# Kernel optimization log

Measured on AMD Instinct MI355X. Metric: run time of the kernel, lower is better.

The kernel has to match this reference:

```python
import jax, jax.numpy as jnp
import numpy as np
from jax import lax

B, HCH, NCODES, H, W = 16, 32, 256, 256, 256

def conv2d(x, w, b, pad):
    y = lax.conv_general_dilated(x, w, (1, 1), [(pad, pad), (pad, pad)],
                                 dimension_numbers=('NCHW', 'OIHW', 'NCHW'))
    return y + b[None, :, None, None]

def vq(z, codebook):
    # z: (B,C,H,W); codebook: (K,C)
    zf = jnp.transpose(z, (0, 2, 3, 1)).reshape(-1, z.shape[1])  # (BHW,C)
    dists = (zf ** 2).sum(1, keepdims=True) + (codebook ** 2).sum(1) - 2.0 * zf @ codebook.T
    idx = jnp.argmin(dists, axis=1)
    zq = codebook[idx].reshape(z.shape[0], z.shape[2], z.shape[3], z.shape[1])
    zq = jnp.transpose(zq, (0, 3, 1, 2))
    # straight-through estimator
    return z + lax.stop_gradient(zq - z)

def setup_inputs() -> dict:
    key = jax.random.key(0)
    ks = jax.random.split(key, 12)
    s = lambda k, shp, scale=0.1: (jax.random.normal(k, shp, jnp.float32) * scale)
    return {
        'x': jax.random.normal(ks[0], (B, 1, H, W), jnp.float32),
        'stem_w': s(ks[1], (HCH, 1, 3, 3)),
        'stem_b': s(ks[2], (HCH,)),
        'up1_w': s(ks[3], (HCH, HCH, 3, 3)),
        'up1_b': s(ks[4], (HCH,)),
        'up2_w': s(ks[5], (HCH, HCH, 1, 1)),
        'up2_b': s(ks[6], (HCH,)),
        'tau_w': s(ks[7], (HCH, HCH, 1, 1)),
        'tau_b': s(ks[8], (HCH,)),
        'codebook': jax.random.uniform(ks[9], (NCODES, HCH), jnp.float32,
                                       -1.0 / NCODES, 1.0 / NCODES),
        'dec_w': s(ks[10], (1, HCH, 1, 1)),
        'dec_b': s(ks[11], (1,)),
        'n_steps': 5,
    }

def reference(x, stem_w, stem_b, up1_w, up1_b, up2_w, up2_b, tau_w, tau_b,
              codebook, dec_w, dec_b, n_steps):
    state = jax.nn.relu(conv2d(x, stem_w, stem_b, 1))
    for t in range(n_steps):
        delta = conv2d(jax.nn.relu(conv2d(state, up1_w, up1_b, 1)), up2_w, up2_b, 0)
        beta = jax.nn.sigmoid(conv2d(state, tau_w, tau_b, 0))
        state = beta * state + (1.0 - beta) * delta
        state = vq(state, codebook)  # vq_every = 1
    return jax.nn.sigmoid(conv2d(state, dec_w, dec_b, 0))
```

## Files before the change

### kernel.cpp

```cpp
#include <hip/hip_runtime.h>
#include <hip/hip_bf16.h>

#define BATCH 16
#define HH 256
#define WW 256
#define NPIX (BATCH*HH*WW)
#define NSTEPS 5
#define CBS 40
#define HS  258
#define HIMG (HS*HS)

#define W1P 0
#define W2P 9216
#define WTP 10240
#define IDP 11264
#define CBP 12288
#define FRAGS_TOT 20480

using u16 = unsigned short;
using u32 = unsigned int;
using u8  = unsigned char;

typedef __attribute__((ext_vector_type(8))) short bf8_t;
typedef __attribute__((ext_vector_type(4))) float f4_t;

#define MFMA16 __builtin_amdgcn_mfma_f32_16x16x32_bf16

#define DPPMIN(v, CTRL) do { \
    u32 _o = (u32)__builtin_amdgcn_update_dpp((int)(v), (int)(v), (CTRL), 0xF, 0xF, false); \
    (v) = _o < (v) ? _o : (v); } while (0)

#define LDS_ORDER() asm volatile("" ::: "memory")

__device__ __forceinline__ float bf2f(u32 u) {
    union { u32 i; float f; } v; v.i = u << 16; return v.f;
}
__device__ __forceinline__ u16 f2bf(float f) {
    union { float f; u32 i; } v; v.f = f;
    u32 x = v.i;
    x += 0x7fffu + ((x >> 16) & 1u);
    return (u16)(x >> 16);
}
__device__ __forceinline__ u32 pack2bf(float a, float b) {
    __hip_bfloat162 h2 = __float22bfloat162_rn(float2{a, b});
    union { __hip_bfloat162 h; u32 u; } v; v.h = h2; return v.u;
}
__device__ __forceinline__ float ldin(const void* p, int i, int f32) {
    return f32 ? ((const float*)p)[i] : bf2f(((const u16*)p)[i]);
}
__device__ __forceinline__ u16 ldbf(const void* p, int i, int f32) {
    return f32 ? f2bf(((const float*)p)[i]) : ((const u16*)p)[i];
}
__device__ __forceinline__ int sniff_f32(const void* xraw) {
    const u32* xw = (const u32*)xraw;
    int cnt = 0;
    for (int j = 0; j < 64; j++) {
        u32 w = xw[j];
        float flo = bf2f(w & 0xffffu);
        float a = fabsf(flo);
        if (flo == 0.0f || (a >= 6e-8f && a <= 64.0f)) cnt++;
    }
    return (cnt < 32) ? 1 : 0;
}
__device__ __forceinline__ int chperm(int kp) { return (kp >> 1) | ((kp & 1) << 4); }

__global__ void prep_kernel(const void* x,
    const void* stem_w, const void* stem_b, const void* up1_w, const void* up1_b,
    const void* up2_w, const void* up2_b, const void* tau_w, const void* tau_b,
    const void* cb, const void* dec_w, const void* dec_b,
    u16* frags, u16* cb_bf, u16* idxh_a, u16* idxh_b,
    float* cn2, float* cadj, float* decdot, float* wf0,
    float* up1_bf, float* up2_bf, float* tau_bf, float* stem_bf, int* flag)
{
    int f32 = sniff_f32(x);
    int i = blockIdx.x * 256 + threadIdx.x;
    if (i == 0) *flag = f32;
    if (i < 9216) {
        int slot = i >> 9, rem = i & 511, lane = rem >> 3, j = rem & 7;
        int tap = slot >> 1, nt = slot & 1;
        int co = nt*16 + (lane & 15), ci = chperm((lane >> 4)*8 + j);
        frags[W1P + i] = ldbf(up1_w, (co*32+ci)*9 + tap, f32);
        return;
    }
    i -= 9216;
    if (i < 1024) {
        int nt = i >> 9, rem = i & 511, lane = rem >> 3, j = rem & 7;
        int co = nt*16 + (lane & 15), k = chperm((lane >> 4)*8 + j);
        frags[W2P + i] = f2bf(-0.25f * ldin(up2_w, co*32 + k, f32));
        return;
    }
    i -= 1024;
    if (i < 1024) {
        int nt = i >> 9, rem = i & 511, lane = rem >> 3, j = rem & 7;
        int co = nt*16 + (lane & 15), k = chperm((lane >> 4)*8 + j);
        frags[WTP + i] = ldbf(tau_w, co*32 + k, f32);
        return;
    }
    i -= 1024;
    if (i < 1024) {
        int s = i >> 9, rem = i & 511, lane = rem >> 3, j = rem & 7;
        int colq = lane & 15, quad = lane >> 4;
        int ch = chperm(quad*8 + j);
        frags[IDP + i] = (ch == (colq + s*16)) ? (u16)0xBE80 : (u16)0;
        return;
    }
    i -= 1024;
    if (i < 8192) {
        int nt = i >> 9, rem = i & 511, lane = rem >> 3, j = rem & 7;
        int code = nt*16 + (lane & 15), c = chperm((lane >> 4)*8 + j);
        frags[CBP + i] = ldbf(cb, code*32 + c, f32);
        return;
    }
    i -= 8192;
    if (i < 257*CBS) {
        int row = i / CBS, p = i - row*CBS;
        cb_bf[i] = (p < 32 && row < 256) ? ldbf(cb, row*32 + chperm(p), f32) : (u16)0;
        return;
    }
    i -= 257*CBS;
    if (i < 16448) {
        int bb = i / 1028, r = i - bb*1028;
        int row, colh;
        if (r < 258)      { row = 0;            colh = r; }
        else if (r < 516) { row = 257;          colh = r - 258; }
        else if (r < 774) { row = r - 516 + 1;  colh = 0; }
        else              { row = r - 774 + 1;  colh = 257; }
        int a = bb*HIMG + row*HS + colh;
        idxh_a[a] = 256; idxh_b[a] = 256;
        return;
    }
    i -= 16448;
    if (i < 256) {
        float s = 0.f;
        for (int c = 0; c < 32; c++) { float v = ldin(cb, i*32+c, f32); s += v*v; }
        cn2[i] = 0.5f * s;
        return;
    }
    i -= 256;
    if (i < 256) {
        float s = 0.f;
        for (int c = 0; c < 32; c++) { float v = ldin(cb, i*32+c, f32); s += v*v; }
        cadj[i] = 0.25f * (0.5f * s) + 0.5f;
        return;
    }
    i -= 256;
    if (i < 256) {
        float s = ldin(dec_b, 0, f32);
        for (int c = 0; c < 32; c++) s += ldin(dec_w, c, f32) * ldin(cb, i*32+c, f32);
        decdot[i] = s;
        return;
    }
    i -= 256;
    if (i < 288) {
        int tap = i >> 5, co = i & 31;
        wf0[i] = ldin(stem_w, co*9 + tap, f32);
        return;
    }
    i -= 288;
    if (i < 32) { up1_bf[i]  = ldin(up1_b, i, f32); return; }
    i -= 32;
    if (i < 32) { up2_bf[i]  = -0.25f * ldin(up2_b, i, f32); return; }
    i -= 32;
    if (i < 32) { tau_bf[i]  = ldin(tau_b, i, f32); return; }
    i -= 32;
    if (i < 32) { stem_bf[i] = ldin(stem_b, i, f32); return; }
}

__global__ __launch_bounds__(256) void step0_kernel(
    const void* __restrict__ xraw, const int* __restrict__ flagp,
    u16* __restrict__ idx_out,
    const u16* __restrict__ fragsg, const float* __restrict__ cn2,
    const float* __restrict__ up1_b, const float* __restrict__ up2_b,
    const float* __restrict__ tau_b, const float* __restrict__ wf0,
    const float* __restrict__ stem_bf)
{
    __shared__ __align__(16) u16 smem[23680];
    u16* w1f   = smem;
    u16* w2f   = smem + 9216;
    u16* wtf   = smem + 10240;
    u16* tileq = smem + 11264;
    u16* hzb   = smem + 21632;
    float* xs  = (float*)hzb;

    const u16* __restrict__ cbg = fragsg + CBP;

    int tid = threadIdx.x;
    int lane = tid & 63, wave = tid >> 6;
    int col = lane & 15, quad = lane >> 4;
    int b = blockIdx.z, x0 = blockIdx.x * 16, y0 = blockIdx.y * 16;

    bf8_t id0 = *(const bf8_t*)&fragsg[IDP + (0*64+lane)*8];
    bf8_t id1 = *(const bf8_t*)&fragsg[IDP + (1*64+lane)*8];

    {
        const uint4* s4 = (const uint4*)(fragsg + W1P);
        uint4* d4 = (uint4*)smem;
        for (int i = tid; i < 1408; i += 256) d4[i] = s4[i];
    }

    {
        int f32 = *flagp;
        for (int pp = tid; pp < 400; pp += 256) {
            int r = pp / 20, c = pp - r*20;
            int gy = y0 - 2 + r, gx = x0 - 2 + c;
            float v = 0.f;
            if ((unsigned)gy < 256u && (unsigned)gx < 256u)
                v = ldin(xraw, (b << 16) | (gy << 8) | gx, f32);
            xs[pp] = v;
        }
        __syncthreads();
        for (int pp = tid; pp < 324; pp += 256) {
            int r = pp / 18, c = pp - r*18;
            int gy = y0 - 1 + r, gx = x0 - 1 + c;
            uint4 qv[4] = {{0,0,0,0},{0,0,0,0},{0,0,0,0},{0,0,0,0}};
            if ((unsigned)gy < 256u && (unsigned)gx < 256u) {
                float acc[32];
#pragma unroll
                for (int co = 0; co < 32; co++) acc[co] = stem_bf[co];
#pragma unroll
                for (int tap = 0; tap < 9; tap++) {
                    float v = xs[(r + tap/3)*20 + (c + tap%3)];
                    const float* w = &wf0[tap*32];
#pragma unroll
                    for (int co = 0; co < 32; co++) acc[co] = fmaf(v, w[co], acc[co]);
                }
                u32* ow = (u32*)qv;
#pragma unroll
                for (int m = 0; m < 16; m++)
                    ow[m] = pack2bf(fmaxf(acc[m], 0.f), fmaxf(acc[m+16], 0.f));
            }
#pragma unroll
            for (int q = 0; q < 4; q++)
                *(uint4*)&tileq[(q*324 + pp)*8] = qv[q];
        }
    }
    __syncthreads();

    float cn2adj[16];
#pragma unroll
    for (int nt = 0; nt < 16; nt++) cn2adj[nt] = 0.25f*cn2[nt*16+col] + 0.5f;
    float bu1C0 = up1_b[col], bu1C1 = up1_b[col+16];
    float bu2_0 = up2_b[col], bu2_1 = up2_b[col+16];
    float bt0 = tau_b[col],   bt1 = tau_b[col+16];
    u16* hzw = &hzb[wave*512];
    u32* hz32 = (u32*)hzw;
    int wy = wave * 4;
    f4_t kz = {0.f,0.f,0.f,0.f};

    bf8_t rows[4][3];
#pragma unroll
    for (int i = 0; i < 4; i++)
#pragma unroll
        for (int dx = 0; dx < 3; dx++)
            rows[i][dx] = *(const bf8_t*)&tileq[(quad*324 + (wy+i)*18 + col+dx)*8];

#pragma unroll
    for (int rrp = 0; rrp < 2; rrp++) {
        if (rrp) {
#pragma unroll
            for (int dx = 0; dx < 3; dx++) {
                rows[0][dx] = rows[2][dx];
                rows[1][dx] = rows[3][dx];
                rows[2][dx] = *(const bf8_t*)&tileq[(quad*324 + (wy+4)*18 + col+dx)*8];
                rows[3][dx] = *(const bf8_t*)&tileq[(quad*324 + (wy+5)*18 + col+dx)*8];
            }
        }
        f4_t aA0 = kz, aA1 = kz, aB0 = kz, aB1 = kz;
#pragma unroll
        for (int t = 0; t < 9; t++) {
            int dy = t/3, dx = t - dy*3;
            bf8_t wA = *(const bf8_t*)&w1f[((t*2+0)*64 + lane)*8];
            bf8_t wB = *(const bf8_t*)&w1f[((t*2+1)*64 + lane)*8];
            aA0 = MFMA16(rows[dy  ][dx], wA, aA0, 0, 0, 0);
            aA1 = MFMA16(rows[dy  ][dx], wB, aA1, 0, 0, 0);
            aB0 = MFMA16(rows[dy+1][dx], wA, aB0, 0, 0, 0);
            aB1 = MFMA16(rows[dy+1][dx], wB, aB1, 0, 0, 0);
        }
#pragma unroll
        for (int r = 0; r < 4; r++) {
            int px = quad*4 + r;
            hz32[px*16 + col] = pack2bf(fmaxf(aA0[r] + bu1C0, 0.f),
                                        fmaxf(aA1[r] + bu1C1, 0.f));
        }
        LDS_ORDER();
        bf8_t hA0 = *(const bf8_t*)&hzw[col*32 + quad*8];
        LDS_ORDER();
#pragma unroll
        for (int r = 0; r < 4; r++) {
            int px = quad*4 + r;
            hz32[px*16 + col] = pack2bf(fmaxf(aB0[r] + bu1C0, 0.f),
                                        fmaxf(aB1[r] + bu1C1, 0.f));
        }
        LDS_ORDER();
        bf8_t hA1 = *(const bf8_t*)&hzw[col*32 + quad*8];
        LDS_ORDER();

        bf8_t w20 = *(const bf8_t*)&w2f[(0*64+lane)*8];
        bf8_t w21 = *(const bf8_t*)&w2f[(1*64+lane)*8];
        bf8_t wt0 = *(const bf8_t*)&wtf[(0*64+lane)*8];
        bf8_t wt1 = *(const bf8_t*)&wtf[(1*64+lane)*8];
        bf8_t sA0 = rows[1][1], sA1 = rows[2][1];
        f4_t d00 = MFMA16(hA0, w20, kz, 0, 0, 0);
        f4_t d01 = MFMA16(hA0, w21, kz, 0, 0, 0);
        f4_t d10 = MFMA16(hA1, w20, kz, 0, 0, 0);
        f4_t d11 = MFMA16(hA1, w21, kz, 0, 0, 0);
        f4_t t00 = MFMA16(sA0, wt0, kz, 0, 0, 0);
        f4_t t01 = MFMA16(sA0, wt1, kz, 0, 0, 0);
        f4_t t10 = MFMA16(sA1, wt0, kz, 0, 0, 0);
        f4_t t11 = MFMA16(sA1, wt1, kz, 0, 0, 0);
        f4_t S0l = MFMA16(sA0, id0, kz, 0, 0, 0);
        f4_t S0h = MFMA16(sA0, id1, kz, 0, 0, 0);
        f4_t S1l = MFMA16(sA1, id0, kz, 0, 0, 0);
        f4_t S1h = MFMA16(sA1, id1, kz, 0, 0, 0);

#pragma unroll
        for (int r = 0; r < 4; r++) {
            int px = quad*4 + r;
            float dl0 = d00[r] + bu2_0, tv0 = t00[r] + bt0;
            float be0 = 1.0f / (1.0f + __expf(-tv0));
            float dl1 = d01[r] + bu2_1, tv1 = t01[r] + bt1;
            float be1 = 1.0f / (1.0f + __expf(-tv1));
            hz32[px*16 + col] = pack2bf(dl0 + be0*(S0l[r] - dl0),
                                        dl1 + be1*(S0h[r] - dl1));
        }
        LDS_ORDER();
        bf8_t zA0 = *(const bf8_t*)&hzw[col*32 + quad*8];
        LDS_ORDER();
#pragma unroll
        for (int r = 0; r < 4; r++) {
            int px = quad*4 + r;
            float dl0 = d10[r] + bu2_0, tv0 = t10[r] + bt0;
            float be0 = 1.0f / (1.0f + __expf(-tv0));
            float dl1 = d11[r] + bu2_1, tv1 = t11[r] + bt1;
            float be1 = 1.0f / (1.0f + __expf(-tv1));
            hz32[px*16 + col] = pack2bf(dl0 + be0*(S1l[r] - dl0),
                                        dl1 + be1*(S1h[r] - dl1));
        }
        LDS_ORDER();
        bf8_t zA1 = *(const bf8_t*)&hzw[col*32 + quad*8];
        LDS_ORDER();

        u32 b0[4], b1[4];
#pragma unroll
        for (int r = 0; r < 4; r++) { b0[r] = 0xFFFFFFFFu; b1[r] = 0xFFFFFFFFu; }
#pragma unroll 4
        for (int nt = 0; nt < 16; nt++) {
            bf8_t cf = *(const bf8_t*)&cbg[(nt*64 + lane)*8];
            f4_t ci = {cn2adj[nt], cn2adj[nt], cn2adj[nt], cn2adj[nt]};
            f4_t s0 = MFMA16(zA0, cf, ci, 0, 0, 0);
            f4_t s1 = MFMA16(zA1, cf, ci, 0, 0, 0);
            u32 code = (u32)(nt*16) | (u32)col;
#pragma unroll
            for (int r = 0; r < 4; r++) {
                u32 k0 = (__builtin_bit_cast(u32, s0[r]) & 0xFFFFFF00u) | code;
                u32 k1 = (__builtin_bit_cast(u32, s1[r]) & 0xFFFFFF00u) | code;
                b0[r] = k0 < b0[r] ? k0 : b0[r];
                b1[r] = k1 < b1[r] ? k1 : b1[r];
            }
        }
#pragma unroll
        for (int r = 0; r < 4; r++) {
            DPPMIN(b0[r], 0x121); DPPMIN(b0[r], 0x122);
            DPPMIN(b0[r], 0x124); DPPMIN(b0[r], 0x128);
            DPPMIN(b1[r], 0x121); DPPMIN(b1[r], 0x122);
            DPPMIN(b1[r], 0x124); DPPMIN(b1[r], 0x128);
        }
        int yr = y0 + wy + rrp*2;
        if (col < 4) {
            int xc = x0 + quad*4 + col + 1;
            idx_out[b*HIMG + (yr+1)*HS + xc] = (u16)(b0[col] & 255u);
            idx_out[b*HIMG + (yr+2)*HS + xc] = (u16)(b1[col] & 255u);
        }
    }
}

__global__ __launch_bounds__(256) void step1_kernel(
    const u16* __restrict__ idx_in, u16* __restrict__ idx_out,
    const u16* __restrict__ fragsg, const u16* __restrict__ cbr_g,
    const float* __restrict__ cadj_g,
    const float* __restrict__ up1_b, const float* __restrict__ up2_b,
    const float* __restrict__ tau_b)
{
    __shared__ __align__(16) u16 smem[24104];
    u16* w1f = smem;
    u16* w2f = smem + 9216;
    u16* wtf = smem + 10240;
    u16* cbr = smem + 11264;
    float* cadjf = (float*)(smem + 21544);
    u16* hzb = smem + 22056;

    int tid = threadIdx.x;
    int lane = tid & 63, wave = tid >> 6;
    int col = lane & 15, quad = lane >> 4;
    int b = blockIdx.z, x0 = blockIdx.x * 16, y0 = blockIdx.y * 32;
    int wy = wave * 4;

    bf8_t id0 = *(const bf8_t*)&fragsg[IDP + (0*64+lane)*8];
    bf8_t id1 = *(const bf8_t*)&fragsg[IDP + (1*64+lane)*8];

    {
        const uint4* s4 = (const uint4*)(fragsg + W1P);
        uint4* d4 = (uint4*)smem;
        for (int i = tid; i < 1408; i += 256) d4[i] = s4[i];
        const uint4* c4 = (const uint4*)cbr_g;
        uint4* e4 = (uint4*)cbr;
        for (int i = tid; i < 1285; i += 256) e4[i] = c4[i];
        const uint4* a4 = (const uint4*)cadj_g;
        uint4* f4p = (uint4*)cadjf;
        if (tid < 64) f4p[tid] = a4[tid];
    }
    __syncthreads();

    float bu1C0 = up1_b[col], bu1C1 = up1_b[col+16];
    float bu2_0 = up2_b[col], bu2_1 = up2_b[col+16];
    float bt0 = tau_b[col],   bt1 = tau_b[col+16];
    u16* hzw = &hzb[wave*512];
    u32* hz32 = (u32*)hzw;
    f4_t kz = {0.f,0.f,0.f,0.f};

    for (int th = 0; th < 2; th++) {
        int yb = y0 + th*16;

        u32 kp[6];
#pragma unroll
        for (int tr = 0; tr < 6; tr++) {
            int base = b*HIMG + (yb + wy + tr)*HS + x0 + col;
            kp[tr] = (u32)idx_in[base]
                   | ((u32)idx_in[base + 1] << 9)
                   | ((u32)idx_in[base + 2] << 18);
        }

        f4_t acc[4][2];
#pragma unroll
        for (int r4 = 0; r4 < 4; r4++) { acc[r4][0] = kz; acc[r4][1] = kz; }
        bf8_t sA[4];
#pragma unroll
        for (int dx = 0; dx < 3; dx++) {
            bf8_t F[6];
#pragma unroll
            for (int tr = 0; tr < 6; tr++) {
                int k = (int)((kp[tr] >> (9*dx)) & 511u);
                F[tr] = *(const bf8_t*)&cbr[k*CBS + quad*8];
            }
            if (dx == 1) {
#pragma unroll
                for (int r4 = 0; r4 < 4; r4++) sA[r4] = F[r4+1];
            }
#pragma unroll
            for (int dy = 0; dy < 3; dy++) {
                int t = dy*3 + dx;
                bf8_t wA = *(const bf8_t*)&w1f[((t*2+0)*64 + lane)*8];
                bf8_t wB = *(const bf8_t*)&w1f[((t*2+1)*64 + lane)*8];
#pragma unroll
                for (int r4 = 0; r4 < 4; r4++) {
                    acc[r4][0] = MFMA16(F[r4+dy], wA, acc[r4][0], 0, 0, 0);
                    acc[r4][1] = MFMA16(F[r4+dy], wB, acc[r4][1], 0, 0, 0);
                }
            }
        }

        bf8_t w20 = *(const bf8_t*)&w2f[(0*64+lane)*8];
        bf8_t w21 = *(const bf8_t*)&w2f[(1*64+lane)*8];
        bf8_t wt0 = *(const bf8_t*)&wtf[(0*64+lane)*8];
        bf8_t wt1 = *(const bf8_t*)&wtf[(1*64+lane)*8];

        bf8_t zA[4];
#pragma unroll
        for (int r4 = 0; r4 < 4; r4++) {
#pragma unroll
            for (int r = 0; r < 4; r++) {
                int px = quad*4 + r;
                hz32[px*16 + col] = pack2bf(fmaxf(acc[r4][0][r] + bu1C0, 0.f),
                                            fmaxf(acc[r4][1][r] + bu1C1, 0.f));
            }
            LDS_ORDER();
            bf8_t hA = *(const bf8_t*)&hzw[col*32 + quad*8];
            LDS_ORDER();
            f4_t d0 = MFMA16(hA, w20, kz, 0, 0, 0);
            f4_t d1 = MFMA16(hA, w21, kz, 0, 0, 0);
            f4_t t0 = MFMA16(sA[r4], wt0, kz, 0, 0, 0);
            f4_t t1 = MFMA16(sA[r4], wt1, kz, 0, 0, 0);
            f4_t Sl = MFMA16(sA[r4], id0, kz, 0, 0, 0);
            f4_t Sh = MFMA16(sA[r4], id1, kz, 0, 0, 0);
#pragma unroll
            for (int r = 0; r < 4; r++) {
                int px = quad*4 + r;
                float dl0 = d0[r] + bu2_0, tv0 = t0[r] + bt0;
                float be0 = 1.0f / (1.0f + __expf(-tv0));
                float dl1 = d1[r] + bu2_1, tv1 = t1[r] + bt1;
                float be1 = 1.0f / (1.0f + __expf(-tv1));
                hz32[px*16 + col] = pack2bf(dl0 + be0*(Sl[r] - dl0),
                                            dl1 + be1*(Sh[r] - dl1));
            }
            LDS_ORDER();
            zA[r4] = *(const bf8_t*)&hzw[col*32 + quad*8];
            LDS_ORDER();
        }

        u32 bk[4][4];
#pragma unroll
        for (int r4 = 0; r4 < 4; r4++)
#pragma unroll
            for (int r = 0; r < 4; r++) bk[r4][r] = 0xFFFFFFFFu;
#pragma unroll
        for (int nt = 0; nt < 16; nt++) {
            bf8_t cf = *(const bf8_t*)&cbr[(nt*16 + col)*CBS + quad*8];
            float ca = cadjf[nt*16 + col];
            f4_t ci = {ca, ca, ca, ca};
            u32 code = (u32)(nt*16) | (u32)col;
#pragma unroll
            for (int r4 = 0; r4 < 4; r4++) {
                f4_t sc = MFMA16(zA[r4], cf, ci, 0, 0, 0);
#pragma unroll
                for (int r = 0; r < 4; r++) {
                    u32 k0 = (__builtin_bit_cast(u32, sc[r]) & 0xFFFFFF00u) | code;
                    bk[r4][r] = k0 < bk[r4][r] ? k0 : bk[r4][r];
                }
            }
        }
#pragma unroll
        for (int r4 = 0; r4 < 4; r4++) {
#pragma unroll
            for (int r = 0; r < 4; r++) {
                DPPMIN(bk[r4][r], 0x121); DPPMIN(bk[r4][r], 0x122);
                DPPMIN(bk[r4][r], 0x124); DPPMIN(bk[r4][r], 0x128);
            }
            int yr = yb + wy + r4;
            if (col < 4)
                idx_out[b*HIMG + (yr+1)*HS + (x0 + quad*4 + col + 1)] =
                    (u16)(bk[r4][col] & 255u);
        }
    }
}

__global__ __launch_bounds__(256) void dec_kernel(const u16* __restrict__ idx,
        const float* __restrict__ decdot, const int* __restrict__ flagp,
        void* __restrict__ out)
{
    int p = blockIdx.x * 256 + threadIdx.x;
    int bb = p >> 16, y = (p >> 8) & 255, xx = p & 255;
    float s = decdot[idx[bb*HIMG + (y+1)*HS + xx + 1]];
    float r = 1.0f / (1.0f + __expf(-s));
    if (*flagp) ((float*)out)[p] = r;
    else        ((u16*)out)[p]   = f2bf(r);
}

extern "C" void kernel_launch(void* const* d_in, const int* in_sizes, int n_in,
                              void* d_out, int out_size, void* d_ws, size_t ws_size,
                              hipStream_t stream)
{
    const void* x      = d_in[0];
    const void* stem_w = d_in[1];
    const void* stem_b = d_in[2];
    const void* up1_w  = d_in[3];
    const void* up1_b  = d_in[4];
    const void* up2_w  = d_in[5];
    const void* up2_b  = d_in[6];
    const void* tau_w  = d_in[7];
    const void* tau_b  = d_in[8];
    const void* cb     = d_in[9];
    const void* dec_w  = d_in[10];
    const void* dec_b  = d_in[11];

    char* ws = (char*)d_ws;
    size_t off = 0;
    auto carve = [&](size_t bytes) -> void* {
        void* p = ws + off;
        off += (bytes + 255) & ~(size_t)255;
        return p;
    };
    u16*   idxA    = (u16*)  carve((size_t)BATCH*HIMG*2);
    u16*   idxB    = (u16*)  carve((size_t)BATCH*HIMG*2);
    u16*   frags   = (u16*)  carve(FRAGS_TOT * 2);
    u16*   cb_bf   = (u16*)  carve(257*CBS * 2);
    float* cn2     = (float*)carve(256 * 4);
    float* cadj    = (float*)carve(256 * 4);
    float* decdot  = (float*)carve(256 * 4);
    float* wf0     = (float*)carve(288 * 4);
    float* up1_bf  = (float*)carve(32 * 4);
    float* up2_bf  = (float*)carve(32 * 4);
    float* tau_bf  = (float*)carve(32 * 4);
    float* stem_bf = (float*)carve(32 * 4);
    int*   flag    = (int*)  carve(4);

    prep_kernel<<<190, 256, 0, stream>>>(x, stem_w, stem_b, up1_w, up1_b,
        up2_w, up2_b, tau_w, tau_b, cb, dec_w, dec_b,
        frags, cb_bf, idxA, idxB, cn2, cadj, decdot, wf0,
        up1_bf, up2_bf, tau_bf, stem_bf, flag);

    dim3 g0(WW/16, HH/16, BATCH);
    step0_kernel<<<g0, 256, 0, stream>>>(x, flag, idxA,
        frags, cn2, up1_bf, up2_bf, tau_bf, wf0, stem_bf);
    dim3 g1(WW/16, HH/32, BATCH);
    u16* cur = idxA; u16* nxt = idxB;
    for (int t = 1; t < NSTEPS; t++) {
        step1_kernel<<<g1, 256, 0, stream>>>(cur, nxt, frags, cb_bf, cadj,
                                             up1_bf, up2_bf, tau_bf);
        u16* tmp = cur; cur = nxt; nxt = tmp;
    }
    dec_kernel<<<NPIX/256, 256, 0, stream>>>(cur, decdot, flag, d_out);
}
```

Before: 394.0 us.

## Fold biases into MFMA accumulators, pack stem FMAs, hoist index loads

Bias adds are moved into the initial MFMA accumulator values, which removes the per-element VALU adds after each matrix op. The stem conv weights and biases are interleaved so that packed two-wide FP32 FMA and max can be used. The codebook-index gathers for both half-tiles are issued before the weight copy to shared memory, so their global latency overlaps that copy. This raises register pressure, since 12 more u32 values and several broadcast vectors stay live.

Measured after the change: 412.2 us. 4.6% more time.

```diff
diff --git a/kernel.cpp b/kernel.cpp
--- a/kernel.cpp
+++ b/kernel.cpp
@@ -23,6 +23,7 @@
 
 typedef __attribute__((ext_vector_type(8))) short bf8_t;
 typedef __attribute__((ext_vector_type(4))) float f4_t;
+typedef __attribute__((ext_vector_type(2))) float f2_t;
 
 #define MFMA16 __builtin_amdgcn_mfma_f32_16x16x32_bf16
 
@@ -152,7 +153,8 @@
     }
     i -= 256;
     if (i < 288) {
-        int tap = i >> 5, co = i & 31;
+        int tap = i >> 5, e = i & 31;
+        int co = (e >> 1) + (e & 1)*16;
         wf0[i] = ldin(stem_w, co*9 + tap, f32);
         return;
     }
@@ -163,7 +165,11 @@
     i -= 32;
     if (i < 32) { tau_bf[i]  = ldin(tau_b, i, f32); return; }
     i -= 32;
-    if (i < 32) { stem_bf[i] = ldin(stem_b, i, f32); return; }
+    if (i < 32) {
+        int co = (i >> 1) + (i & 1)*16;
+        stem_bf[i] = ldin(stem_b, co, f32);
+        return;
+    }
 }
 
 __global__ __launch_bounds__(256) void step0_kernel(
@@ -209,25 +215,31 @@
             xs[pp] = v;
         }
         __syncthreads();
+        const f2_t* wb2 = (const f2_t*)stem_bf;
         for (int pp = tid; pp < 324; pp += 256) {
             int r = pp / 18, c = pp - r*18;
             int gy = y0 - 1 + r, gx = x0 - 1 + c;
             uint4 qv[4] = {{0,0,0,0},{0,0,0,0},{0,0,0,0},{0,0,0,0}};
             if ((unsigned)gy < 256u && (unsigned)gx < 256u) {
-                float acc[32];
-#pragma unroll
-                for (int co = 0; co < 32; co++) acc[co] = stem_bf[co];
+                f2_t acc2[16];
+#pragma unroll
+                for (int m = 0; m < 16; m++) acc2[m] = wb2[m];
 #pragma unroll
                 for (int tap = 0; tap < 9; tap++) {
                     float v = xs[(r + tap/3)*20 + (c + tap%3)];
-                    const float* w = &wf0[tap*32];
-#pragma unroll
-                    for (int co = 0; co < 32; co++) acc[co] = fmaf(v, w[co], acc[co]);
+                    f2_t vv = {v, v};
+                    const f2_t* w2 = (const f2_t*)&wf0[tap*32];
+#pragma unroll
+                    for (int m = 0; m < 16; m++)
+                        acc2[m] = __builtin_elementwise_fma(vv, w2[m], acc2[m]);
                 }
                 u32* ow = (u32*)qv;
-#pragma unroll
-                for (int m = 0; m < 16; m++)
-                    ow[m] = pack2bf(fmaxf(acc[m], 0.f), fmaxf(acc[m+16], 0.f));
+                f2_t z2 = {0.f, 0.f};
+#pragma unroll
+                for (int m = 0; m < 16; m++) {
+                    f2_t h2 = __builtin_elementwise_max(acc2[m], z2);
+                    ow[m] = pack2bf(h2[0], h2[1]);
+                }
             }
 #pragma unroll
             for (int q = 0; q < 4; q++)
@@ -242,6 +254,12 @@
     float bu1C0 = up1_b[col], bu1C1 = up1_b[col+16];
     float bu2_0 = up2_b[col], bu2_1 = up2_b[col+16];
     float bt0 = tau_b[col],   bt1 = tau_b[col+16];
+    f4_t cb1A = {bu1C0, bu1C0, bu1C0, bu1C0};
+    f4_t cb1B = {bu1C1, bu1C1, bu1C1, bu1C1};
+    f4_t cb2_0 = {bu2_0, bu2_0, bu2_0, bu2_0};
+    f4_t cb2_1 = {bu2_1, bu2_1, bu2_1, bu2_1};
+    f4_t cbt0 = {bt0, bt0, bt0, bt0};
+    f4_t cbt1 = {bt1, bt1, bt1, bt1};
     u16* hzw = &hzb[wave*512];
     u32* hz32 = (u32*)hzw;
     int wy = wave * 4;
@@ -265,7 +283,7 @@
                 rows[3][dx] = *(const bf8_t*)&tileq[(quad*324 + (wy+5)*18 + col+dx)*8];
             }
         }
-        f4_t aA0 = kz, aA1 = kz, aB0 = kz, aB1 = kz;
+        f4_t aA0 = cb1A, aA1 = cb1B, aB0 = cb1A, aB1 = cb1B;
 #pragma unroll
         for (int t = 0; t < 9; t++) {
             int dy = t/3, dx = t - dy*3;
@@ -279,8 +297,7 @@
 #pragma unroll
         for (int r = 0; r < 4; r++) {
             int px = quad*4 + r;
-            hz32[px*16 + col] = pack2bf(fmaxf(aA0[r] + bu1C0, 0.f),
-                                        fmaxf(aA1[r] + bu1C1, 0.f));
+            hz32[px*16 + col] = pack2bf(fmaxf(aA0[r], 0.f), fmaxf(aA1[r], 0.f));
         }
         LDS_ORDER();
         bf8_t hA0 = *(const bf8_t*)&hzw[col*32 + quad*8];
@@ -288,8 +305,7 @@
 #pragma unroll
         for (int r = 0; r < 4; r++) {
             int px = quad*4 + r;
-            hz32[px*16 + col] = pack2bf(fmaxf(aB0[r] + bu1C0, 0.f),
-                                        fmaxf(aB1[r] + bu1C1, 0.f));
+            hz32[px*16 + col] = pack2bf(fmaxf(aB0[r], 0.f), fmaxf(aB1[r], 0.f));
         }
         LDS_ORDER();
         bf8_t hA1 = *(const bf8_t*)&hzw[col*32 + quad*8];
@@ -300,14 +316,14 @@
         bf8_t wt0 = *(const bf8_t*)&wtf[(0*64+lane)*8];
         bf8_t wt1 = *(const bf8_t*)&wtf[(1*64+lane)*8];
         bf8_t sA0 = rows[1][1], sA1 = rows[2][1];
-        f4_t d00 = MFMA16(hA0, w20, kz, 0, 0, 0);
-        f4_t d01 = MFMA16(hA0, w21, kz, 0, 0, 0);
-        f4_t d10 = MFMA16(hA1, w20, kz, 0, 0, 0);
-        f4_t d11 = MFMA16(hA1, w21, kz, 0, 0, 0);
-        f4_t t00 = MFMA16(sA0, wt0, kz, 0, 0, 0);
-        f4_t t01 = MFMA16(sA0, wt1, kz, 0, 0, 0);
-        f4_t t10 = MFMA16(sA1, wt0, kz, 0, 0, 0);
-        f4_t t11 = MFMA16(sA1, wt1, kz, 0, 0, 0);
+        f4_t d00 = MFMA16(hA0, w20, cb2_0, 0, 0, 0);
+        f4_t d01 = MFMA16(hA0, w21, cb2_1, 0, 0, 0);
+        f4_t d10 = MFMA16(hA1, w20, cb2_0, 0, 0, 0);
+        f4_t d11 = MFMA16(hA1, w21, cb2_1, 0, 0, 0);
+        f4_t t00 = MFMA16(sA0, wt0, cbt0, 0, 0, 0);
+        f4_t t01 = MFMA16(sA0, wt1, cbt1, 0, 0, 0);
+        f4_t t10 = MFMA16(sA1, wt0, cbt0, 0, 0, 0);
+        f4_t t11 = MFMA16(sA1, wt1, cbt1, 0, 0, 0);
         f4_t S0l = MFMA16(sA0, id0, kz, 0, 0, 0);
         f4_t S0h = MFMA16(sA0, id1, kz, 0, 0, 0);
         f4_t S1l = MFMA16(sA1, id0, kz, 0, 0, 0);
@@ -316,9 +332,9 @@
 #pragma unroll
         for (int r = 0; r < 4; r++) {
             int px = quad*4 + r;
-            float dl0 = d00[r] + bu2_0, tv0 = t00[r] + bt0;
+            float dl0 = d00[r], tv0 = t00[r];
             float be0 = 1.0f / (1.0f + __expf(-tv0));
-            float dl1 = d01[r] + bu2_1, tv1 = t01[r] + bt1;
+            float dl1 = d01[r], tv1 = t01[r];
             float be1 = 1.0f / (1.0f + __expf(-tv1));
             hz32[px*16 + col] = pack2bf(dl0 + be0*(S0l[r] - dl0),
                                         dl1 + be1*(S0h[r] - dl1));
@@ -329,9 +345,9 @@
 #pragma unroll
         for (int r = 0; r < 4; r++) {
             int px = quad*4 + r;
-            float dl0 = d10[r] + bu2_0, tv0 = t10[r] + bt0;
+            float dl0 = d10[r], tv0 = t10[r];
             float be0 = 1.0f / (1.0f + __expf(-tv0));
-            float dl1 = d11[r] + bu2_1, tv1 = t11[r] + bt1;
+            float dl1 = d11[r], tv1 = t11[r];
             float be1 = 1.0f / (1.0f + __expf(-tv1));
             hz32[px*16 + col] = pack2bf(dl0 + be0*(S1l[r] - dl0),
                                         dl1 + be1*(S1h[r] - dl1));
@@ -398,6 +414,17 @@
     bf8_t id0 = *(const bf8_t*)&fragsg[IDP + (0*64+lane)*8];
     bf8_t id1 = *(const bf8_t*)&fragsg[IDP + (1*64+lane)*8];
 
+    u32 kps[2][6];
+#pragma unroll
+    for (int th = 0; th < 2; th++)
+#pragma unroll
+        for (int tr = 0; tr < 6; tr++) {
+            int base = b*HIMG + (y0 + th*16 + wy + tr)*HS + x0 + col;
+            kps[th][tr] = (u32)idx_in[base]
+                        | ((u32)idx_in[base + 1] << 9)
+                        | ((u32)idx_in[base + 2] << 18);
+        }
+
     {
         const uint4* s4 = (const uint4*)(fragsg + W1P);
         uint4* d4 = (uint4*)smem;
@@ -414,25 +441,24 @@
     float bu1C0 = up1_b[col], bu1C1 = up1_b[col+16];
     float bu2_0 = up2_b[col], bu2_1 = up2_b[col+16];
     float bt0 = tau_b[col],   bt1 = tau_b[col+16];
+    f4_t cb1A = {bu1C0, bu1C0, bu1C0, bu1C0};
+    f4_t cb1B = {bu1C1, bu1C1, bu1C1, bu1C1};
+    f4_t cb2_0 = {bu2_0, bu2_0, bu2_0, bu2_0};
+    f4_t cb2_1 = {bu2_1, bu2_1, bu2_1, bu2_1};
+    f4_t cbt0 = {bt0, bt0, bt0, bt0};
+    f4_t cbt1 = {bt1, bt1, bt1, bt1};
     u16* hzw = &hzb[wave*512];
     u32* hz32 = (u32*)hzw;
     f4_t kz = {0.f,0.f,0.f,0.f};
 
+#pragma unroll
     for (int th = 0; th < 2; th++) {
         int yb = y0 + th*16;
-
-        u32 kp[6];
-#pragma unroll
-        for (int tr = 0; tr < 6; tr++) {
-            int base = b*HIMG + (yb + wy + tr)*HS + x0 + col;
-            kp[tr] = (u32)idx_in[base]
-                   | ((u32)idx_in[base + 1] << 9)
-                   | ((u32)idx_in[base + 2] << 18);
-        }
+        const u32* kp = kps[th];
 
         f4_t acc[4][2];
 #pragma unroll
-        for (int r4 = 0; r4 < 4; r4++) { acc[r4][0] = kz; acc[r4][1] = kz; }
+        for (int r4 = 0; r4 < 4; r4++) { acc[r4][0] = cb1A; acc[r4][1] = cb1B; }
         bf8_t sA[4];
 #pragma unroll
         for (int dx = 0; dx < 3; dx++) {
@@ -470,24 +496,24 @@
 #pragma unroll
             for (int r = 0; r < 4; r++) {
                 int px = quad*4 + r;
-                hz32[px*16 + col] = pack2bf(fmaxf(acc[r4][0][r] + bu1C0, 0.f),
-                                            fmaxf(acc[r4][1][r] + bu1C1, 0.f));
+                hz32[px*16 + col] = pack2bf(fmaxf(acc[r4][0][r], 0.f),
+                                            fmaxf(acc[r4][1][r], 0.f));
             }
             LDS_ORDER();
             bf8_t hA = *(const bf8_t*)&hzw[col*32 + quad*8];
             LDS_ORDER();
-            f4_t d0 = MFMA16(hA, w20, kz, 0, 0, 0);
-            f4_t d1 = MFMA16(hA, w21, kz, 0, 0, 0);
-            f4_t t0 = MFMA16(sA[r4], wt0, kz, 0, 0, 0);
-            f4_t t1 = MFMA16(sA[r4], wt1, kz, 0, 0, 0);
+            f4_t d0 = MFMA16(hA, w20, cb2_0, 0, 0, 0);
+            f4_t d1 = MFMA16(hA, w21, cb2_1, 0, 0, 0);
+            f4_t t0 = MFMA16(sA[r4], wt0, cbt0, 0, 0, 0);
+            f4_t t1 = MFMA16(sA[r4], wt1, cbt1, 0, 0, 0);
             f4_t Sl = MFMA16(sA[r4], id0, kz, 0, 0, 0);
             f4_t Sh = MFMA16(sA[r4], id1, kz, 0, 0, 0);
 #pragma unroll
             for (int r = 0; r < 4; r++) {
                 int px = quad*4 + r;
-                float dl0 = d0[r] + bu2_0, tv0 = t0[r] + bt0;
+                float dl0 = d0[r], tv0 = t0[r];
                 float be0 = 1.0f / (1.0f + __expf(-tv0));
-                float dl1 = d1[r] + bu2_1, tv1 = t1[r] + bt1;
+                float dl1 = d1[r], tv1 = t1[r];
                 float be1 = 1.0f / (1.0f + __expf(-tv1));
                 hz32[px*16 + col] = pack2bf(dl0 + be0*(Sl[r] - dl0),
                                             dl1 + be1*(Sh[r] - dl1));
```
